# Optimization experiments

Hardware: AMD Instinct MI355X
Metric: run time of the kernel (lower is better)

Reference implementation:

```python
import jax, jax.numpy as jnp
import numpy as np


def _lstm_bi(x, wih, whh, b):
    # x: [B,T,D]; wih: [2,D,4H]; whh: [2,H,4H]; b: [2,4H]. PyTorch gate order i,f,g,o.
    def run(xs, wi, wh, bb):
        B, H = xs.shape[1], wh.shape[0]
        def step(carry, xt):
            h, c = carry
            g = xt @ wi + h @ wh + bb
            i, f, gg, o = jnp.split(g, 4, axis=-1)
            c = jax.nn.sigmoid(f) * c + jax.nn.sigmoid(i) * jnp.tanh(gg)
            h = jax.nn.sigmoid(o) * jnp.tanh(c)
            return (h, c), h
        z0 = jnp.zeros((B, H), xs.dtype)
        _, hs = jax.lax.scan(step, (z0, z0), xs)
        return hs
    xs = jnp.swapaxes(x, 0, 1)  # [T,B,D]
    hf = run(xs, wih[0], whh[0], b[0])
    hb = run(xs[::-1], wih[1], whh[1], b[1])[::-1]
    return jnp.swapaxes(jnp.concatenate([hf, hb], axis=-1), 0, 1)


def _norm_thr(att, thr):
    # sum-normalize, threshold-sparsify, renormalize (PSP core)
    att = att / (jnp.sum(att, -1, keepdims=True) + 1e-8)
    att = jnp.where(att > thr, att, jnp.zeros_like(att))
    return att / (jnp.sum(att, -1, keepdims=True) + 1e-8)


def _ln(x, g, b):
    mu = jnp.mean(x, -1, keepdims=True)
    var = jnp.mean(jnp.square(x - mu), -1, keepdims=True)
    return (x - mu) / jnp.sqrt(var + 1e-6) * g + b


def _forward(audio, video, thr_val, fa_w1, fa_w2, av_aw, av_ab, av_vw, av_vb,
             av_v2w, av_gw, av_hw, fv_w1, fv_w2, la_wih, la_whh, la_b,
             lv_wih, lv_whh, lv_b, vL1, vL2, aL1, aL2, vfc, afc, ln_g, ln_b, L1w, L2w):
    bs, T = audio.shape[0], audio.shape[1]
    fa = (audio @ fa_w1) @ fa_w2                          # [B,T,128]
    vf = video.reshape(bs, T, -1, video.shape[-1])        # [B,T,49,512]
    # AVGA audio-guided visual attention
    v_h = jax.nn.relu(vf @ av_vw + av_vb)                 # [B,T,49,512]
    a_h = jax.nn.relu(fa @ av_aw + av_ab)                 # [B,T,512]
    content = v_h @ av_v2w + (a_h @ av_gw)[..., None]     # [B,T,49,49]
    z = jnp.squeeze(jnp.tanh(content) @ av_hw, -1)        # [B,T,49]
    alpha = jax.nn.softmax(z, -1)
    video_t = jnp.einsum('btp,btpd->btd', alpha, vf)      # [B,T,512]
    video_t = (video_t @ fv_w1) @ fv_w2                   # [B,T,128]
    # bidirectional LSTMs
    lstm_a = _lstm_bi(fa, la_wih, la_whh, la_b)           # [B,T,256]
    lstm_v = _lstm_bi(video_t, lv_wih, lv_whh, lv_b)      # [B,T,256]
    # PSP (eval mode: dropout is identity)
    v_b1 = jax.nn.relu(lstm_v @ vL1)
    v_b2 = jax.nn.relu(lstm_v @ vL2)
    a_b1 = jax.nn.relu(lstm_a @ aL1)
    a_b2 = jax.nn.relu(lstm_a @ aL2)
    scale = 1.0 / jnp.sqrt(jnp.asarray(v_b2.shape[-1], v_b2.dtype))
    att = jax.nn.relu(jnp.einsum('bvd,bad->bva', v_b2, a_b1) * scale)  # v->a raw
    att_v2a = _norm_thr(att, thr_val)
    att_a2v = _norm_thr(jnp.swapaxes(att, 1, 2), thr_val)
    v_psp = lstm_v + jnp.einsum('bva,bad->bvd', att_v2a, a_b2)
    a_psp = lstm_a + jnp.einsum('bav,bvd->bad', att_a2v, v_b1)
    v_psp = _ln(jax.nn.relu(v_psp @ vfc), ln_g, ln_b)
    a_psp = _ln(jax.nn.relu(a_psp @ afc), ln_g, ln_b)
    fuse = 0.5 * (v_psp + a_psp)
    vn = v_psp / jnp.maximum(jnp.linalg.norm(v_psp, axis=-1, keepdims=True), 1e-12)
    an = a_psp / jnp.maximum(jnp.linalg.norm(a_psp, axis=-1, keepdims=True), 1e-12)
    cross_att = jnp.sum(vn * an, -1)                      # [B,T]
    out = jax.nn.relu(fuse @ L1w) @ L2w                   # [B,T,29]
    return (fuse, out, cross_att)


def setup_inputs() -> dict:
    key = jax.random.key(0)
    ks = iter(jax.random.split(key, 40))
    def w(*shape):
        fan_in = shape[-2] if len(shape) > 1 else shape[-1]
        return jax.random.normal(next(ks), shape, jnp.float32) * (1.0 / np.sqrt(fan_in))
    B, T = 256, 10
    return dict(
        audio=jax.random.normal(next(ks), (B, T, 128), jnp.float32),
        video=jax.random.normal(next(ks), (B, T, 7, 7, 512), jnp.float32),
        thr_val=jnp.float32(0.099),
        fa_w1=w(128, 256), fa_w2=w(256, 128),
        av_aw=w(128, 512), av_ab=jnp.zeros((512,), jnp.float32),
        av_vw=w(512, 512), av_vb=jnp.zeros((512,), jnp.float32),
        av_v2w=w(512, 49), av_gw=w(512, 49), av_hw=w(49, 1),
        fv_w1=w(512, 256), fv_w2=w(256, 128),
        la_wih=w(2, 128, 512), la_whh=w(2, 128, 512), la_b=jnp.zeros((2, 512), jnp.float32),
        lv_wih=w(2, 128, 512), lv_whh=w(2, 128, 512), lv_b=jnp.zeros((2, 512), jnp.float32),
        vL1=w(256, 256), vL2=w(256, 256), aL1=w(256, 256), aL2=w(256, 256),
        vfc=w(256, 256), afc=w(256, 256),
        ln_g=jnp.ones((256,), jnp.float32), ln_b=jnp.zeros((256,), jnp.float32),
        L1w=w(256, 64), L2w=w(64, 29),
    )


def reference(audio, video, thr_val, fa_w1, fa_w2, av_aw, av_ab, av_vw, av_vb,
              av_v2w, av_gw, av_hw, fv_w1, fv_w2, la_wih, la_whh, la_b,
              lv_wih, lv_whh, lv_b, vL1, vL2, aL1, aL2, vfc, afc, ln_g, ln_b, L1w, L2w):
    return _forward(audio, video, thr_val, fa_w1, fa_w2, av_aw, av_ab, av_vw, av_vb,
                    av_v2w, av_gw, av_hw, fv_w1, fv_w2, la_wih, la_whh, la_b,
                    lv_wih, lv_whh, lv_b, vL1, vL2, aL1, aL2, vfc, afc, ln_g, ln_b, L1w, L2w)
```

## Files before the change

### kernel.cpp

```cpp
#include <hip/hip_runtime.h>
#include <math.h>

#define DEV __device__ __forceinline__

typedef _Float16 f16x8 __attribute__((ext_vector_type(8)));
typedef _Float16 f16x4 __attribute__((ext_vector_type(4)));
typedef float    f32x4 __attribute__((ext_vector_type(4)));

DEV float sigmoidf_(float x){ return 1.0f/(1.0f + expf(-x)); }

DEV float wred64(float x){
    #pragma unroll
    for (int off=32; off; off>>=1) x += __shfl_xor(x, off);
    return x;
}

#define MFMA16(a,b,c) __builtin_amdgcn_mfma_f32_16x16x32_f16(a,b,c,0,0,0)

DEV void packone(const float* __restrict__ src, int N, int NfrTot, int nfOff,
                 _Float16* __restrict__ Dh, _Float16* __restrict__ Dl, int o){
    int j = o&7, l16 = (o>>3)&15, kg = (o>>7)&3;
    int rest = o>>9;
    int nfl = rest % (N>>4), kt = rest / (N>>4);
    int k = kt*32 + kg*8 + j, n = nfl*16 + l16;
    float x = src[(size_t)k*N + n];
    _Float16 h = (_Float16)x;
    size_t d = ((size_t)kt*NfrTot + nfOff + nfl)*512 + kg*128 + l16*8 + j;
    Dh[d] = h; Dl[d] = (_Float16)(x - (float)h);
}

__global__ __launch_bounds__(256) void k_prep(
    const float* __restrict__ fa_w1, const float* __restrict__ fa_w2, float* __restrict__ faW,
    const float* __restrict__ fv_w1, const float* __restrict__ fv_w2,
    const float* __restrict__ av_vw, _Float16* __restrict__ Bh, _Float16* __restrict__ Bl,
    const float* __restrict__ v2w, _Float16* __restrict__ Wh, _Float16* __restrict__ Wl,
    const float* __restrict__ lv_wih,
    _Float16* __restrict__ PKfv_h, _Float16* __restrict__ PKfv_l,
    _Float16* __restrict__ PKxv_h, _Float16* __restrict__ PKxv_l)
{
    int bid = blockIdx.x, t = threadIdx.x;
    if (bid < 64){
        int idx = bid*256+t; int m = idx>>7, n = idx&127;
        float acc=0.f;
        for (int k=0;k<256;k++) acc += fa_w1[m*256+k]*fa_w2[k*128+n];
        faW[idx]=acc;
    } else if (bid < 1088){
        int o = (bid-64)*256+t;
        int j = o & 7, l16 = (o>>3)&15, kg = (o>>7)&3, nf = (o>>9)&31, kt = o>>14;
        int k = kt*32 + kg*8 + j, n = nf*16 + l16;
        float x = av_vw[(size_t)k*512 + n];
        _Float16 h = (_Float16)x;
        Bh[o] = h; Bl[o] = (_Float16)(x - (float)h);
    } else if (bid < 1216){
        int o = (bid-1088)*256+t;
        int j = o & 7, l16 = (o>>3)&15, kg = (o>>7)&3, qf = (o>>9)&3, kbg = o>>11;
        int k = kbg*32 + kg*8 + j, q = qf*16 + l16;
        float x = (q < 49) ? v2w[(size_t)k*49 + q] : 0.f;
        _Float16 h = (_Float16)x;
        Wh[o] = h; Wl[o] = (_Float16)(x - (float)h);
    } else if (bid < 1472){
        int o = (bid-1216)*256+t;
        int j=o&7, l16=(o>>3)&15, kg=(o>>7)&3; int rest=o>>9;
        int nfl = rest&7, kt = rest>>3;
        int k = kt*32+kg*8+j, n = nfl*16+l16;
        float acc=0.f;
        for (int kk=0;kk<256;kk++) acc += fv_w1[k*256+kk]*fv_w2[kk*128+n];
        _Float16 h=(_Float16)acc;
        size_t d = ((size_t)kt*8 + nfl)*512 + kg*128 + l16*8 + j;
        PKfv_h[d]=h; PKfv_l[d]=(_Float16)(acc-(float)h);
    } else {
        int seg = (bid-1472)>>8;
        int o = ((bid-1472)&255)*256+t;
        packone(lv_wih + (size_t)seg*65536, 512, 64, seg*32, PKxv_h, PKxv_l, o);
    }
}

__global__ __launch_bounds__(256) void k_faga2(
    const float* __restrict__ audio, const float* __restrict__ faW,
    const float* __restrict__ av_aw, const float* __restrict__ av_ab,
    const float* __restrict__ av_gw,
    const float* __restrict__ la_wih, const float* __restrict__ la_b,
    float* __restrict__ gGA, float* __restrict__ xpA)
{
    int b0 = blockIdx.x*8; int t = threadIdx.x;
    __shared__ float sau[8][128], sfa[8][128], sah[8][512];
    for (int i=t;i<1024;i+=256){ int bt=i>>7,k=i&127; sau[bt][k]=audio[(size_t)(b0+bt)*128+k]; }
    __syncthreads();
    for (int u=0;u<4;u++){
        int i=t+u*256, bt=i>>7, n=i&127;
        float acc=0.f;
        for (int k4=0;k4<32;k4++){
            float4 x4=*(const float4*)&sau[bt][k4*4];
            acc+=x4.x*faW[(k4*4)*128+n]+x4.y*faW[(k4*4+1)*128+n]
                +x4.z*faW[(k4*4+2)*128+n]+x4.w*faW[(k4*4+3)*128+n];
        }
        sfa[bt][n]=acc;
    }
    __syncthreads();
    for (int u=0;u<2;u++){
        int n=t+u*256;
        float bv=av_ab[n];
        float acc[8]={bv,bv,bv,bv,bv,bv,bv,bv};
        for (int k4=0;k4<32;k4++){
            float w0=av_aw[(k4*4)*512+n], w1=av_aw[(k4*4+1)*512+n],
                  w2=av_aw[(k4*4+2)*512+n], w3=av_aw[(k4*4+3)*512+n];
            #pragma unroll
            for (int bt=0;bt<8;bt++){
                float4 x4=*(const float4*)&sfa[bt][k4*4];
                acc[bt]+=x4.x*w0+x4.y*w1+x4.z*w2+x4.w*w3;
            }
        }
        #pragma unroll
        for (int bt=0;bt<8;bt++) sah[bt][n]=fmaxf(acc[bt],0.f);
    }
    __syncthreads();
    for (int hh=0;hh<2;hh++){
        if (t<196){
            int bt=hh*4 + t/49, q=t%49;
            float acc=0.f;
            for (int k=0;k<512;k++) acc+=sah[bt][k]*av_gw[k*49+q];
            gGA[(size_t)(b0+bt)*49+q]=acc;
        }
    }
    for (int u=0;u<4;u++){
        int n = t + u*256;
        int dir = n >> 9, g = n & 511;
        const float* W = la_wih + (size_t)dir*65536;
        float bvv = la_b[dir*512 + g];
        float acc[8] = {bvv,bvv,bvv,bvv,bvv,bvv,bvv,bvv};
        for (int k4=0;k4<32;k4++){
            float w0=W[(k4*4+0)*512+g], w1=W[(k4*4+1)*512+g],
                  w2=W[(k4*4+2)*512+g], w3=W[(k4*4+3)*512+g];
            #pragma unroll
            for (int bt=0;bt<8;bt++){
                float4 x4=*(const float4*)&sfa[bt][k4*4];
                acc[bt]+=x4.x*w0+x4.y*w1+x4.z*w2+x4.w*w3;
            }
        }
        #pragma unroll
        for (int bt=0;bt<8;bt++)
            xpA[((size_t)(b0+bt))*1024 + n] = acc[bt];
    }
}

DEV void cvt4_(float4 v, f16x4& hv, f16x4& lv){
    hv[0]=(_Float16)v.x; lv[0]=(_Float16)(v.x-(float)hv[0]);
    hv[1]=(_Float16)v.y; lv[1]=(_Float16)(v.y-(float)hv[1]);
    hv[2]=(_Float16)v.z; lv[2]=(_Float16)(v.z-(float)hv[2]);
    hv[3]=(_Float16)v.w; lv[3]=(_Float16)(v.w-(float)hv[3]);
}

__global__ __launch_bounds__(256,2) void k_avga_fused(
    const float* __restrict__ video,
    const _Float16* __restrict__ Bh, const _Float16* __restrict__ Bl,
    const float* __restrict__ bias,
    const _Float16* __restrict__ Wh, const _Float16* __restrict__ Wl,
    const float* __restrict__ gGA, const float* __restrict__ hw,
    float* __restrict__ vT)
{
    __shared__ __align__(16) char smem[67072];
    int bt = blockIdx.x;
    int t = threadIdx.x;
    int lane = t & 63, w = t >> 6;
    int l16 = lane & 15, lq = lane >> 4;
    int lb = lane * 16;

    int am = t >> 3, ak = (t & 7) * 4;
    int aoff1 = ((am>>4)*4 + (ak>>3))*256 + (am&15)*16 + (ak&7)*2;
    int am2 = am + 32;
    int aoff2 = ((am2>>4)*4 + (ak>>3))*256 + (am2&15)*16 + (ak&7)*2;
    size_t r1 = (size_t)bt*49 + am;  if (r1 > 125439) r1 = 125439;
    size_t r2 = (size_t)bt*49 + am2; if (r2 > 125439) r2 = 125439;
    const float* Arow1 = video + r1*512 + ak;
    const float* Arow2 = video + r2*512 + ak;

    const f32x4 vzero = {0.f,0.f,0.f,0.f};
    f32x4 acc[4][8];
    #pragma unroll
    for (int p=0;p<4;p++)
        #pragma unroll
        for (int q=0;q<8;q++) acc[p][q] = vzero;

    float4 paA0, paA1, paB0, paB1;
    paA0 = *(const float4*)(Arow1);
    paA1 = *(const float4*)(Arow2);
    paB0 = *(const float4*)(Arow1 + 32);
    paB1 = *(const float4*)(Arow2 + 32);
    {
        f16x4 hv, lv;
        char* h0 = &smem[0];
        cvt4_(paA0, hv, lv);
        *(f16x4*)(h0 + aoff1) = hv; *(f16x4*)(h0 + 4096 + aoff1) = lv;
        cvt4_(paA1, hv, lv);
        *(f16x4*)(h0 + aoff2) = hv; *(f16x4*)(h0 + 4096 + aoff2) = lv;
        char* h1 = &smem[8192];
        cvt4_(paB0, hv, lv);
        *(f16x4*)(h1 + aoff1) = hv; *(f16x4*)(h1 + 4096 + aoff1) = lv;
        cvt4_(paB1, hv, lv);
        *(f16x4*)(h1 + aoff2) = hv; *(f16x4*)(h1 + 4096 + aoff2) = lv;
    }
    __syncthreads();

    for (int skt = 0; skt < 8; ++skt){
        int cur2 = (skt & 1) * 2;
        bool more = (skt < 7);
        if (more){
            int ko = (skt+1)*64;
            paA0 = *(const float4*)(Arow1 + ko);
            paA1 = *(const float4*)(Arow2 + ko);
            paB0 = *(const float4*)(Arow1 + ko + 32);
            paB1 = *(const float4*)(Arow2 + ko + 32);
        }
        #pragma unroll
        for (int kk=0; kk<2; ++kk){
            int kt = skt*2 + kk;
            const char* aB = &smem[(cur2+kk)*8192];
            f16x8 ah[4], al[4];
            #pragma unroll
            for (int p=0;p<4;p++){
                ah[p] = *(const f16x8*)(aB + p*1024 + lb);
                al[p] = *(const f16x8*)(aB + 4096 + p*1024 + lb);
            }
            #pragma unroll
            for (int q=0;q<8;q++){
                size_t bo = (size_t)kt*16384 + (size_t)(w*8 + q)*512 + lane*8;
                f16x8 bh  = *(const f16x8*)(Bh + bo);
                f16x8 bl2 = *(const f16x8*)(Bl + bo);
                #pragma unroll
                for (int p=0;p<4;p++){
                    acc[p][q] = MFMA16(ah[p], bh,  acc[p][q]);
                    acc[p][q] = MFMA16(ah[p], bl2, acc[p][q]);
                    acc[p][q] = MFMA16(al[p], bh,  acc[p][q]);
                }
            }
        }
        if (more){
            f16x4 hv, lv;
            char* h0 = &smem[(cur2^2)*8192];
            cvt4_(paA0, hv, lv);
            *(f16x4*)(h0 + aoff1) = hv; *(f16x4*)(h0 + 4096 + aoff1) = lv;
            cvt4_(paA1, hv, lv);
            *(f16x4*)(h0 + aoff2) = hv; *(f16x4*)(h0 + 4096 + aoff2) = lv;
            char* h1 = &smem[((cur2^2)+1)*8192];
            cvt4_(paB0, hv, lv);
            *(f16x4*)(h1 + aoff1) = hv; *(f16x4*)(h1 + 4096 + aoff1) = lv;
            cvt4_(paB1, hv, lv);
            *(f16x4*)(h1 + aoff2) = hv; *(f16x4*)(h1 + 4096 + aoff2) = lv;
        }
        __syncthreads();
    }

    float bv[8];
    #pragma unroll
    for (int q=0;q<8;q++) bv[q] = bias[w*128 + q*16 + l16];

    char* vh = &smem[w*8192];
    f32x4 cacc[4][4];
    #pragma unroll
    for (int p=0;p<4;p++)
        #pragma unroll
        for (int qf=0;qf<4;qf++) cacc[p][qf] = vzero;

    #pragma unroll
    for (int c=0;c<4;c++){
        #pragma unroll
        for (int p=0;p<4;p++)
            #pragma unroll
            for (int qq=0;qq<2;qq++){
                int q = c*2 + qq;
                int offbase = p*1024 + (qq*2 + (l16>>3))*256 + (l16&7)*2;
                #pragma unroll
                for (int r=0;r<4;r++){
                    float x = fmaxf(acc[p][q][r] + bv[q], 0.f);
                    _Float16 hh = (_Float16)x;
                    _Float16 ll = (_Float16)(x - (float)hh);
                    int off = offbase + (lq*4 + r)*16;
                    *(_Float16*)(vh + off)        = hh;
                    *(_Float16*)(vh + 4096 + off) = ll;
                }
            }
        int kbg = w*4 + c;
        f16x8 vhh[4], vhl[4];
        #pragma unroll
        for (int p=0;p<4;p++){
            vhh[p] = *(const f16x8*)(vh + p*1024 + lb);
            vhl[p] = *(const f16x8*)(vh + 4096 + p*1024 + lb);
        }
        #pragma unroll
        for (int qf=0;qf<4;qf++){
            size_t wo = (size_t)kbg*2048 + qf*512 + lane*8;
            f16x8 wh = *(const f16x8*)(Wh + wo);
            f16x8 wl = *(const f16x8*)(Wl + wo);
            #pragma unroll
            for (int p=0;p<4;p++){
                cacc[p][qf] = MFMA16(vhh[p], wh, cacc[p][qf]);
                cacc[p][qf] = MFMA16(vhh[p], wl, cacc[p][qf]);
                cacc[p][qf] = MFMA16(vhl[p], wh, cacc[p][qf]);
            }
        }
    }

    __syncthreads();
    float* pw = (float*)&smem[w*16384];
    #pragma unroll
    for (int p=0;p<4;p++)
        #pragma unroll
        for (int qf=0;qf<4;qf++)
            #pragma unroll
            for (int r=0;r<4;r++)
                pw[(p*16 + lq*4 + r)*64 + qf*16 + l16] = cacc[p][qf][r];
    __syncthreads();
    float* cb = (float*)&smem[0];
    for (int i=t; i<4096; i+=256)
        cb[i] = cb[i] + cb[4096+i] + cb[8192+i] + cb[12288+i];
    __syncthreads();

    float* szp    = (float*)&smem[65536];
    float* salpha = (float*)&smem[66560];
    if (t < 196){
        int p = t >> 2, ds = t & 3;
        float ga = gGA[(size_t)bt*49 + p];
        float part = 0.f;
        for (int q = ds*13; q < ds*13+13 && q < 49; q++)
            part += tanhf(cb[p*64 + q] + ga) * hw[q];
        szp[t] = part;
    }
    __syncthreads();
    if (t < 64){
        float z = (t<49) ? (szp[t*4]+szp[t*4+1]+szp[t*4+2]+szp[t*4+3]) : -1e30f;
        float m = z;
        #pragma unroll
        for (int off=32; off; off>>=1) m = fmaxf(m, __shfl_xor(m, off));
        float e = (t<49)? expf(z - m) : 0.f;
        float s = e;
        #pragma unroll
        for (int off=32; off; off>>=1) s += __shfl_xor(s, off);
        salpha[t] = e / s;
    }
    __syncthreads();
    const float* vb = video + (size_t)bt*49*512;
    #pragma unroll
    for (int u=0;u<2;u++){
        int d = t + u*256;
        float a0 = 0.f;
        for (int p=0;p<49;p++) a0 += salpha[p] * vb[(size_t)p*512 + d];
        vT[(size_t)bt*512 + d] = a0;
    }
}

__global__ __launch_bounds__(256) void k_gemm2(
    const float* __restrict__ vT,
    const _Float16* __restrict__ Fh, const _Float16* __restrict__ Fl,
    const _Float16* __restrict__ Xh, const _Float16* __restrict__ Xl,
    const float* __restrict__ lv_b,
    float* __restrict__ xpV)
{
    __shared__ __align__(16) char sA[2][4096];
    __shared__ float sV[32][132];
    int t = threadIdx.x, lane = t&63, w = t>>6;
    int l16 = lane&15, lq = lane>>4, lb = lane*16;
    int row0 = blockIdx.x * 32;

    int am = t>>3, ak = (t&7)*4;
    int aoff = ((am>>4)*4 + (ak>>3))*256 + (am&15)*16 + (ak&7)*2;
    const float* Arow = vT + (size_t)(row0+am)*512 + ak;

    const f32x4 vzero = {0.f,0.f,0.f,0.f};
    f32x4 acc1[2][2];
    #pragma unroll
    for (int p=0;p<2;p++)
        #pragma unroll
        for (int q=0;q<2;q++) acc1[p][q] = vzero;

    float4 pa = *(const float4*)(Arow);
    {
        f16x4 hv, lv;
        char* h = &sA[0][0];
        cvt4_(pa, hv, lv);
        *(f16x4*)(h + aoff) = hv; *(f16x4*)(h + 2048 + aoff) = lv;
    }
    __syncthreads();
    for (int kt = 0; kt < 16; ++kt){
        int cur = kt & 1;
        bool more = (kt < 15);
        if (more) pa = *(const float4*)(Arow + (kt+1)*32);
        const char* aB = &sA[cur][0];
        f16x8 ah[2], al[2];
        #pragma unroll
        for (int p=0;p<2;p++){
            ah[p] = *(const f16x8*)(aB + p*1024 + lb);
            al[p] = *(const f16x8*)(aB + 2048 + p*1024 + lb);
        }
        #pragma unroll
        for (int q=0;q<2;q++){
            size_t bo = ((size_t)kt*8 + w*2 + q)*512 + lane*8;
            f16x8 bh  = *(const f16x8*)(Fh + bo);
            f16x8 bl2 = *(const f16x8*)(Fl + bo);
            #pragma unroll
            for (int p=0;p<2;p++){
                acc1[p][q] = MFMA16(ah[p], bh,  acc1[p][q]);
                acc1[p][q] = MFMA16(ah[p], bl2, acc1[p][q]);
                acc1[p][q] = MFMA16(al[p], bh,  acc1[p][q]);
            }
        }
        if (more){
            char* h = &sA[cur^1][0];
            f16x4 hv, lv;
            cvt4_(pa, hv, lv);
            *(f16x4*)(h + aoff) = hv; *(f16x4*)(h + 2048 + aoff) = lv;
        }
        __syncthreads();
    }
    #pragma unroll
    for (int q=0;q<2;q++){
        int n = (w*2+q)*16 + l16;
        #pragma unroll
        for (int p=0;p<2;p++)
            #pragma unroll
            for (int r=0;r<4;r++)
                sV[p*16 + lq*4 + r][n] = acc1[p][q][r];
    }
    __syncthreads();

    int nf0 = blockIdx.y*16 + w*4;
    f32x4 acc2[2][4];
    #pragma unroll
    for (int p=0;p<2;p++)
        #pragma unroll
        for (int q=0;q<4;q++) acc2[p][q] = vzero;

    pa = *(const float4*)&sV[am][ak];
    {
        f16x4 hv, lv;
        char* h = &sA[0][0];
        cvt4_(pa, hv, lv);
        *(f16x4*)(h + aoff) = hv; *(f16x4*)(h + 2048 + aoff) = lv;
    }
    __syncthreads();
    for (int kt = 0; kt < 4; ++kt){
        int cur = kt & 1;
        bool more = (kt < 3);
        if (more) pa = *(const float4*)&sV[am][(kt+1)*32 + ak];
        const char* aB = &sA[cur][0];
        f16x8 ah[2], al[2];
        #pragma unroll
        for (int p=0;p<2;p++){
            ah[p] = *(const f16x8*)(aB + p*1024 + lb);
            al[p] = *(const f16x8*)(aB + 2048 + p*1024 + lb);
        }
        #pragma unroll
        for (int q=0;q<4;q++){
            size_t bo = ((size_t)kt*64 + nf0 + q)*512 + lane*8;
            f16x8 bh  = *(const f16x8*)(Xh + bo);
            f16x8 bl2 = *(const f16x8*)(Xl + bo);
            #pragma unroll
            for (int p=0;p<2;p++){
                acc2[p][q] = MFMA16(ah[p], bh,  acc2[p][q]);
                acc2[p][q] = MFMA16(ah[p], bl2, acc2[p][q]);
                acc2[p][q] = MFMA16(al[p], bh,  acc2[p][q]);
            }
        }
        if (more){
            char* h = &sA[cur^1][0];
            f16x4 hv, lv;
            cvt4_(pa, hv, lv);
            *(f16x4*)(h + aoff) = hv; *(f16x4*)(h + 2048 + aoff) = lv;
        }
        __syncthreads();
    }
    #pragma unroll
    for (int q=0;q<4;q++){
        int n = (nf0+q)*16 + l16;
        float bv = lv_b[n];
        #pragma unroll
        for (int p=0;p<2;p++){
            #pragma unroll
            for (int r=0;r<4;r++)
                xpV[(size_t)(row0 + p*16 + lq*4 + r)*1024 + n] = acc2[p][q][r] + bv;
        }
    }
}

__global__ __launch_bounds__(256) void k_lstm(
    const float* __restrict__ xpA, const float* __restrict__ xpV,
    const float* __restrict__ la_whh, const float* __restrict__ lv_whh,
    float* __restrict__ lstm_a, float* __restrict__ lstm_v)
{
    int blk = blockIdx.x;
    int c = blk >> 6;
    int chunk = blk & 63;
    int t = threadIdx.x;
    int j  = t & 127;
    int bh = t >> 7;
    const float* whh = ((c<2)? la_whh : lv_whh) + (size_t)(c&1)*128*512;
    const float* xpm = (c<2)? xpA : xpV;
    float* outp = (c<2)? lstm_a : lstm_v;
    int dir = c & 1;

    __shared__ float hbuf[4][128];
    float cc[2] = {0.f,0.f};
    for (int i=t;i<512;i+=256) ((float*)hbuf)[i] = 0.f;
    __syncthreads();

    for (int s=0; s<10; s++){
        int tt = dir ? (9-s) : s;
        float gi[2], gf[2], gg[2], go[2];
        #pragma unroll
        for (int b=0;b<2;b++){
            int gb = chunk*4 + bh*2 + b;
            const float* xrow = xpm + ((size_t)gb*10 + tt)*1024 + dir*512;
            gi[b]=xrow[j]; gf[b]=xrow[128+j]; gg[b]=xrow[256+j]; go[b]=xrow[384+j];
        }
        #pragma unroll 4
        for (int k=0;k<128;k++){
            float wi = whh[k*512 + j];
            float wf = whh[k*512 + 128 + j];
            float wg = whh[k*512 + 256 + j];
            float wo = whh[k*512 + 384 + j];
            #pragma unroll
            for (int b=0;b<2;b++){
                float hk = hbuf[bh*2+b][k];
                gi[b] += hk*wi; gf[b] += hk*wf; gg[b] += hk*wg; go[b] += hk*wo;
            }
        }
        __syncthreads();
        #pragma unroll
        for (int b=0;b<2;b++){
            float i_ = sigmoidf_(gi[b]);
            float f_ = sigmoidf_(gf[b]);
            float g_ = tanhf(gg[b]);
            float o_ = sigmoidf_(go[b]);
            cc[b] = f_*cc[b] + i_*g_;
            float h_ = o_*tanhf(cc[b]);
            hbuf[bh*2+b][j] = h_;
            int gb = chunk*4 + bh*2 + b;
            outp[((size_t)gb*10 + tt)*256 + dir*128 + j] = h_;
        }
        __syncthreads();
    }
}

__global__ __launch_bounds__(256) void k_tail(
    const float* __restrict__ lstm_a, const float* __restrict__ lstm_v,
    const float* __restrict__ vL1, const float* __restrict__ vL2,
    const float* __restrict__ aL1, const float* __restrict__ aL2,
    const float* __restrict__ vfc, const float* __restrict__ afc,
    const float* __restrict__ thrp,
    const float* __restrict__ ln_g, const float* __restrict__ ln_b,
    const float* __restrict__ L1w, const float* __restrict__ L2w,
    float* __restrict__ dout)
{
    int b = blockIdx.x, t = threadIdx.x;
    int lane = t & 63, w = t >> 6;
    __shared__ float sla[10][256], slv[10][256];
    __shared__ float sb1v[10][256], sb2v[10][256], sb1a[10][256], sb2a[10][256];
    __shared__ float sfu[10][256];
    __shared__ float s64[10][64];
    __shared__ float satt[100], s_v2a[100], s_a2v[100];
    __shared__ float sredp[160];
    __shared__ float scos[120];

    size_t base = (size_t)b*2560;
    for (int i=t;i<2560;i+=256){
        ((float*)sla)[i] = lstm_a[base+i];
        ((float*)slv)[i] = lstm_v[base+i];
    }
    __syncthreads();

    {
        float a1[10], a2[10];
        #pragma unroll
        for (int r=0;r<10;r++){ a1[r]=0.f; a2[r]=0.f; }
        #pragma unroll 4
        for (int k=0;k<256;k++){
            float w1 = vL1[k*256+t], w2 = vL2[k*256+t];
            #pragma unroll
            for (int r=0;r<10;r++){ float x=slv[r][k]; a1[r]+=x*w1; a2[r]+=x*w2; }
        }
        #pragma unroll
        for (int r=0;r<10;r++){ sb1v[r][t]=fmaxf(a1[r],0.f); sb2v[r][t]=fmaxf(a2[r],0.f); }
        #pragma unroll
        for (int r=0;r<10;r++){ a1[r]=0.f; a2[r]=0.f; }
        #pragma unroll 4
        for (int k=0;k<256;k++){
            float w1 = aL1[k*256+t], w2 = aL2[k*256+t];
            #pragma unroll
            for (int r=0;r<10;r++){ float x=sla[r][k]; a1[r]+=x*w1; a2[r]+=x*w2; }
        }
        #pragma unroll
        for (int r=0;r<10;r++){ sb1a[r][t]=fmaxf(a1[r],0.f); sb2a[r][t]=fmaxf(a2[r],0.f); }
    }
    __syncthreads();

    if (t < 100){
        int v = t/10, a = t - v*10;
        float acc=0.f;
        for (int k=0;k<256;k++) acc += sb2v[v][k]*sb1a[a][k];
        satt[t] = fmaxf(acc*(1.0f/16.0f), 0.f);
    }
    __syncthreads();
    float thr = thrp[0];
    if (t < 10){
        int v = t;
        float rs=0.f; for(int a=0;a<10;a++) rs += satt[v*10+a];
        float inv = 1.f/(rs+1e-8f);
        float tmp[10]; float rs2=0.f;
        for(int a=0;a<10;a++){ float x = satt[v*10+a]*inv; x = (x>thr)?x:0.f; tmp[a]=x; rs2+=x; }
        float inv2 = 1.f/(rs2+1e-8f);
        for(int a=0;a<10;a++) s_v2a[v*10+a] = tmp[a]*inv2;
    } else if (t>=16 && t<26){
        int a = t-16;
        float cs=0.f; for(int v=0;v<10;v++) cs += satt[v*10+a];
        float inv = 1.f/(cs+1e-8f);
        float tmp[10]; float cs2=0.f;
        for(int v=0;v<10;v++){ float x = satt[v*10+a]*inv; x=(x>thr)?x:0.f; tmp[v]=x; cs2+=x; }
        float inv2 = 1.f/(cs2+1e-8f);
        for(int v=0;v<10;v++) s_a2v[a*10+v] = tmp[v]*inv2;
    }
    __syncthreads();

    #pragma unroll
    for (int v=0;v<10;v++){
        float acc = slv[v][t];
        #pragma unroll
        for (int a=0;a<10;a++) acc += s_v2a[v*10+a]*sb2a[a][t];
        slv[v][t] = acc;
    }
    #pragma unroll
    for (int a=0;a<10;a++){
        float acc = sla[a][t];
        #pragma unroll
        for (int v=0;v<10;v++) acc += s_a2v[a*10+v]*sb1v[v][t];
        sla[a][t] = acc;
    }
    __syncthreads();

    float fv[10], fa2[10];
    #pragma unroll
    for (int r=0;r<10;r++){ fv[r]=0.f; fa2[r]=0.f; }
    #pragma unroll 4
    for (int k=0;k<256;k++){
        float wv = vfc[k*256+t], wa = afc[k*256+t];
        #pragma unroll
        for (int r=0;r<10;r++){ fv[r]+=slv[r][k]*wv; fa2[r]+=sla[r][k]*wa; }
    }
    #pragma unroll
    for (int r=0;r<10;r++){ fv[r]=fmaxf(fv[r],0.f); fa2[r]=fmaxf(fa2[r],0.f); }

    #pragma unroll
    for (int r=0;r<10;r++){
        float s1 = wred64(fv[r]);
        float s2 = wred64(fv[r]*fv[r]);
        float s3 = wred64(fa2[r]);
        float s4 = wred64(fa2[r]*fa2[r]);
        if (lane==0){
            sredp[r*16 + 0*4 + w] = s1; sredp[r*16 + 1*4 + w] = s2;
            sredp[r*16 + 2*4 + w] = s3; sredp[r*16 + 3*4 + w] = s4;
        }
    }
    __syncthreads();
    float gt = ln_g[t], bt2 = ln_b[t];
    #pragma unroll
    for (int r=0;r<10;r++){
        float s1 = sredp[r*16+0]+sredp[r*16+1]+sredp[r*16+2]+sredp[r*16+3];
        float s2 = sredp[r*16+4]+sredp[r*16+5]+sredp[r*16+6]+sredp[r*16+7];
        float s3 = sredp[r*16+8]+sredp[r*16+9]+sredp[r*16+10]+sredp[r*16+11];
        float s4 = sredp[r*16+12]+sredp[r*16+13]+sredp[r*16+14]+sredp[r*16+15];
        float muv = s1*(1.f/256.f);
        float varv = s2*(1.f/256.f) - muv*muv;
        float rsv = 1.f/sqrtf(varv+1e-6f);
        float vln = (fv[r]-muv)*rsv*gt + bt2;
        float mua = s3*(1.f/256.f);
        float vara = s4*(1.f/256.f) - mua*mua;
        float rsa = 1.f/sqrtf(vara+1e-6f);
        float aln = (fa2[r]-mua)*rsa*gt + bt2;
        float fu = 0.5f*(vln+aln);
        dout[(size_t)(b*10+r)*256 + t] = fu;
        sfu[r][t] = fu;
        float c1 = wred64(vln*vln);
        float c2 = wred64(aln*aln);
        float c3 = wred64(vln*aln);
        if (lane==0){
            scos[r*12 + 0*4 + w] = c1; scos[r*12 + 1*4 + w] = c2; scos[r*12 + 2*4 + w] = c3;
        }
    }
    __syncthreads();
    if (t < 10){
        int r = t;
        float nv2 = scos[r*12+0]+scos[r*12+1]+scos[r*12+2]+scos[r*12+3];
        float na2 = scos[r*12+4]+scos[r*12+5]+scos[r*12+6]+scos[r*12+7];
        float dva = scos[r*12+8]+scos[r*12+9]+scos[r*12+10]+scos[r*12+11];
        float nv = fmaxf(sqrtf(nv2), 1e-12f);
        float na = fmaxf(sqrtf(na2), 1e-12f);
        dout[729600 + b*10 + r] = dva/(nv*na);
    }

    #pragma unroll
    for (int pass=0; pass<3; ++pass){
        int r = pass*4 + w;
        if (r < 10){
            float acc = 0.f;
            for (int k4=0;k4<64;k4++){
                float4 f4 = *(const float4*)&sfu[r][k4*4];
                acc += f4.x*L1w[(k4*4)*64+lane] + f4.y*L1w[(k4*4+1)*64+lane]
                     + f4.z*L1w[(k4*4+2)*64+lane] + f4.w*L1w[(k4*4+3)*64+lane];
            }
            s64[r][lane] = fmaxf(acc, 0.f);
        }
    }
    __syncthreads();
    for (int i=t; i<290; i+=256){
        int r = i/29, jj = i - r*29;
        float acc = 0.f;
        #pragma unroll
        for (int k=0;k<64;k++) acc += s64[r][k]*L2w[k*29+jj];
        dout[655360 + (size_t)(b*10+r)*29 + jj] = acc;
    }
}

extern "C" void kernel_launch(void* const* d_in, const int* in_sizes, int n_in,
                              void* d_out, int out_size, void* d_ws, size_t ws_size,
                              hipStream_t stream) {
    const float* audio  = (const float*)d_in[0];
    const float* video  = (const float*)d_in[1];
    const float* thrp   = (const float*)d_in[2];
    const float* fa_w1  = (const float*)d_in[3];
    const float* fa_w2  = (const float*)d_in[4];
    const float* av_aw  = (const float*)d_in[5];
    const float* av_ab  = (const float*)d_in[6];
    const float* av_vw  = (const float*)d_in[7];
    const float* av_vb  = (const float*)d_in[8];
    const float* av_v2w = (const float*)d_in[9];
    const float* av_gw  = (const float*)d_in[10];
    const float* av_hw  = (const float*)d_in[11];
    const float* fv_w1  = (const float*)d_in[12];
    const float* fv_w2  = (const float*)d_in[13];
    const float* la_wih = (const float*)d_in[14];
    const float* la_whh = (const float*)d_in[15];
    const float* la_b   = (const float*)d_in[16];
    const float* lv_wih = (const float*)d_in[17];
    const float* lv_whh = (const float*)d_in[18];
    const float* lv_b   = (const float*)d_in[19];
    const float* vL1    = (const float*)d_in[20];
    const float* vL2    = (const float*)d_in[21];
    const float* aL1    = (const float*)d_in[22];
    const float* aL2    = (const float*)d_in[23];
    const float* vfc    = (const float*)d_in[24];
    const float* afc    = (const float*)d_in[25];
    const float* ln_g   = (const float*)d_in[26];
    const float* ln_b   = (const float*)d_in[27];
    const float* L1w    = (const float*)d_in[28];
    const float* L2w    = (const float*)d_in[29];
    float* dout = (float*)d_out;
    float* ws = (float*)d_ws;

    float* faW  = ws;
    float* gGA  = ws + 409600;
    float* vT   = ws + 535040;
    float* xpA  = ws + 2173440;
    float* xpV  = ws + 4794880;
    float* la   = ws + 7416320;
    float* lv   = ws + 8071680;
    _Float16* Bh = (_Float16*)(ws + 12659200);
    _Float16* Bl = (_Float16*)(ws + 12790272);
    _Float16* Wh = (_Float16*)(ws + 12921344);
    _Float16* Wl = (_Float16*)(ws + 12937728);
    _Float16* PKfv_h = (_Float16*)(ws + 12954112);
    _Float16* PKfv_l = (_Float16*)(ws + 12986880);
    _Float16* PKxv_h = (_Float16*)(ws + 13150720);
    _Float16* PKxv_l = (_Float16*)(ws + 13216256);

    k_prep<<<1984, 256, 0, stream>>>(fa_w1, fa_w2, faW, fv_w1, fv_w2,
                                     av_vw, Bh, Bl, av_v2w, Wh, Wl,
                                     lv_wih, PKfv_h, PKfv_l, PKxv_h, PKxv_l);
    k_faga2<<<320, 256, 0, stream>>>(audio, faW, av_aw, av_ab, av_gw,
                                     la_wih, la_b, gGA, xpA);
    k_avga_fused<<<2560, 256, 0, stream>>>(video, Bh, Bl, av_vb, Wh, Wl,
                                           gGA, av_hw, vT);
    k_gemm2<<<dim3(80,4), 256, 0, stream>>>(vT, PKfv_h, PKfv_l,
                                            PKxv_h, PKxv_l, lv_b, xpV);
    k_lstm<<<256, 256, 0, stream>>>(xpA, xpV, la_whh, lv_whh, la, lv);
    k_tail<<<256, 256, 0, stream>>>(la, lv, vL1, vL2, aL1, aL2, vfc, afc,
                                    thrp, ln_g, ln_b, L1w, L2w, dout);
}
```

Before: 668.5 us.

## Replace double-buffered A staging with two bulk phases of eight K-tiles

The A-operand staging in the video projection GEMM is restructured. The old loop prefetched the next 64-wide K chunk into registers and converted it into the alternate shared-memory buffer while MFMAs ran, synchronising on every step. The new version loads and converts half of K (eight 32-wide tiles, 64 KB of LDS) at once, synchronises, then runs the MFMAs for those tiles, doing this twice. This cuts barriers from eight to four per block, but global loads no longer overlap compute.

```diff
diff --git a/kernel.cpp b/kernel.cpp
--- a/kernel.cpp
+++ b/kernel.cpp
@@ -181,40 +181,22 @@
         #pragma unroll
         for (int q=0;q<8;q++) acc[p][q] = vzero;
 
-    float4 paA0, paA1, paB0, paB1;
-    paA0 = *(const float4*)(Arow1);
-    paA1 = *(const float4*)(Arow2);
-    paB0 = *(const float4*)(Arow1 + 32);
-    paB1 = *(const float4*)(Arow2 + 32);
-    {
-        f16x4 hv, lv;
-        char* h0 = &smem[0];
-        cvt4_(paA0, hv, lv);
-        *(f16x4*)(h0 + aoff1) = hv; *(f16x4*)(h0 + 4096 + aoff1) = lv;
-        cvt4_(paA1, hv, lv);
-        *(f16x4*)(h0 + aoff2) = hv; *(f16x4*)(h0 + 4096 + aoff2) = lv;
-        char* h1 = &smem[8192];
-        cvt4_(paB0, hv, lv);
-        *(f16x4*)(h1 + aoff1) = hv; *(f16x4*)(h1 + 4096 + aoff1) = lv;
-        cvt4_(paB1, hv, lv);
-        *(f16x4*)(h1 + aoff2) = hv; *(f16x4*)(h1 + 4096 + aoff2) = lv;
-    }
-    __syncthreads();
-
-    for (int skt = 0; skt < 8; ++skt){
-        int cur2 = (skt & 1) * 2;
-        bool more = (skt < 7);
-        if (more){
-            int ko = (skt+1)*64;
-            paA0 = *(const float4*)(Arow1 + ko);
-            paA1 = *(const float4*)(Arow2 + ko);
-            paB0 = *(const float4*)(Arow1 + ko + 32);
-            paB1 = *(const float4*)(Arow2 + ko + 32);
-        }
-        #pragma unroll
-        for (int kk=0; kk<2; ++kk){
-            int kt = skt*2 + kk;
-            const char* aB = &smem[(cur2+kk)*8192];
+    for (int ph = 0; ph < 2; ++ph){
+        for (int kl = 0; kl < 8; ++kl){
+            int ko = ph*256 + kl*32;
+            float4 a0 = *(const float4*)(Arow1 + ko);
+            float4 a1 = *(const float4*)(Arow2 + ko);
+            char* h = &smem[kl*8192];
+            f16x4 hv, lv;
+            cvt4_(a0, hv, lv);
+            *(f16x4*)(h + aoff1) = hv; *(f16x4*)(h + 4096 + aoff1) = lv;
+            cvt4_(a1, hv, lv);
+            *(f16x4*)(h + aoff2) = hv; *(f16x4*)(h + 4096 + aoff2) = lv;
+        }
+        __syncthreads();
+        for (int kl = 0; kl < 8; ++kl){
+            int kt = ph*8 + kl;
+            const char* aB = &smem[kl*8192];
             f16x8 ah[4], al[4];
             #pragma unroll
             for (int p=0;p<4;p++){
@@ -233,19 +215,6 @@
                     acc[p][q] = MFMA16(al[p], bh,  acc[p][q]);
                 }
             }
-        }
-        if (more){
-            f16x4 hv, lv;
-            char* h0 = &smem[(cur2^2)*8192];
-            cvt4_(paA0, hv, lv);
-            *(f16x4*)(h0 + aoff1) = hv; *(f16x4*)(h0 + 4096 + aoff1) = lv;
-            cvt4_(paA1, hv, lv);
-            *(f16x4*)(h0 + aoff2) = hv; *(f16x4*)(h0 + 4096 + aoff2) = lv;
-            char* h1 = &smem[((cur2^2)+1)*8192];
-            cvt4_(paB0, hv, lv);
-            *(f16x4*)(h1 + aoff1) = hv; *(f16x4*)(h1 + 4096 + aoff1) = lv;
-            cvt4_(paB1, hv, lv);
-            *(f16x4*)(h1 + aoff2) = hv; *(f16x4*)(h1 + 4096 + aoff2) = lv;
         }
         __syncthreads();
     }
```

After: 709.0 us. 1.06x slower.
